# Optimization experiments

Measured on AMD Instinct MI355X. Metric: run time of the kernel, lower is better.

Reference implementation:

```python
import jax, jax.numpy as jnp
import numpy as np

PROTO_DIM = 512
PROTO_NUM = 4096
BSZ = 256
SUBTEXT_NUM = 64
TEMP = 0.9


def setup_inputs() -> dict:
    key = jax.random.key(0)
    k1, k2, k3 = jax.random.split(key, 3)
    subtexts = jax.random.normal(k1, (BSZ, SUBTEXT_NUM, PROTO_DIM), dtype=jnp.float32)
    prototype = jax.random.normal(k2, (PROTO_NUM, PROTO_DIM), dtype=jnp.float32)
    uniform = jax.random.uniform(k3, (BSZ * SUBTEXT_NUM, PROTO_NUM), dtype=jnp.float32)
    return {"subtexts": subtexts, "prototype": prototype, "uniform": uniform}


def reference(subtexts, prototype, uniform):
    # flatten: [N, D] with N = bsz * subtext_num
    flatten = subtexts.reshape(-1, PROTO_DIM)
    # dist: [N, proto_num] = flatten @ prototype.T
    dist = jnp.einsum("nd,pd->np", flatten, prototype)
    # Gumbel noise g = -log(-log(u)), matching torch F.gumbel_softmax sampling
    tiny = jnp.float32(1e-10)
    gumbel = -jnp.log(-jnp.log(uniform + tiny) + tiny)
    # noisy logits -> softmax over codebook dim (tau = curr_temp)
    soft_one_hot = jax.nn.softmax((dist + gumbel) / jnp.float32(TEMP), axis=1)
    # output: [N, D] soft codebook lookup
    output = jnp.einsum("np,pd->nd", soft_one_hot, prototype)
    proto_idx = jnp.argmax(soft_one_hot, axis=1)
    proto_loss = jnp.mean(jnp.abs(output - flatten))
    return (output, proto_loss, proto_idx)
```

## Files before the change

kernel.cpp:

```cpp
#include <hip/hip_runtime.h>
#include <math.h>

#define NROWS 16384
#define DIM   512
#define NPROTO 4096
#define TINV (1.0f / 0.9f)
#define LOSS_OFF ((size_t)NROWS * DIM)
#define IDX_OFF  ((size_t)NROWS * DIM + 1)

typedef __attribute__((ext_vector_type(8))) short short8;
typedef __attribute__((ext_vector_type(4))) float f32x4;

__global__ void zero_loss_kernel(float* out) { out[LOSS_OFF] = 0.0f; }

static __device__ __forceinline__ unsigned short f2bf(float x) {
    unsigned u = __float_as_uint(x);
    u = (u + 0x7fffu + ((u >> 16) & 1u)) >> 16;
    return (unsigned short)u;
}
static __device__ __forceinline__ float bf2f(unsigned short b) {
    return __uint_as_float(((unsigned)b) << 16);
}
static __device__ __forceinline__ void gl_lds16(const void* g, void* l) {
    __builtin_amdgcn_global_load_lds((const __attribute__((address_space(1))) unsigned int*)g,
                                     (__attribute__((address_space(3))) unsigned int*)l, 16, 0, 0);
}

__global__ __launch_bounds__(256)
void split_bf16_kernel(const float* __restrict__ src, unsigned short* __restrict__ dhi,
                       unsigned short* __restrict__ dmid, int nrows)
{
    __shared__ __align__(16) unsigned short shi[64][520];
    __shared__ __align__(16) unsigned short smid[64][520];
    const int tid = threadIdx.x;
    const int r0 = blockIdx.x * 64;
#pragma unroll
    for (int q = 0; q < 32; ++q) {
        int idx = q * 256 + tid;
        int row = idx >> 7;
        int k4 = (idx & 127) << 2;
        float4 v = *(const float4*)&src[(size_t)(r0 + row) * DIM + k4];
        unsigned short h0 = f2bf(v.x), h1 = f2bf(v.y), h2 = f2bf(v.z), h3 = f2bf(v.w);
        shi[row][k4] = h0; shi[row][k4 + 1] = h1; shi[row][k4 + 2] = h2; shi[row][k4 + 3] = h3;
        smid[row][k4]     = f2bf(v.x - bf2f(h0));
        smid[row][k4 + 1] = f2bf(v.y - bf2f(h1));
        smid[row][k4 + 2] = f2bf(v.z - bf2f(h2));
        smid[row][k4 + 3] = f2bf(v.w - bf2f(h3));
    }
    __syncthreads();
    const int row = tid & 63;
#pragma unroll
    for (int i = 0; i < 16; ++i) {
        int c = i * 4 + (tid >> 6);
        size_t o = (size_t)c * nrows + r0 + row;
        ((ulonglong2*)dhi)[o]  = *(const ulonglong2*)&shi[row][c * 8];
        ((ulonglong2*)dmid)[o] = *(const ulonglong2*)&smid[row][c * 8];
    }
}

#define BM 32
#define BN 256
#define NCHUNK (NPROTO / BN)
#define NT 16
#define CAP 80
#define PRUNE_AT 56
#define THRH 12.0f

__global__ __launch_bounds__(256, 2)
void attr_proto_mfma(const float* __restrict__ A, const float* __restrict__ Pr,
                     const float* __restrict__ U, float* __restrict__ out,
                     const unsigned short* __restrict__ wsAhi, const unsigned short* __restrict__ wsAmid,
                     const unsigned short* __restrict__ wsPhi, const unsigned short* __restrict__ wsPmid)
{
    __shared__ __align__(16) unsigned short sA[2][4][BM][8];
    __shared__ __align__(16) unsigned short sP[2][4][BN][8];
    __shared__ float hZ[BM][CAP];
    __shared__ unsigned short hI[BM][CAP];
    __shared__ int cnt[BM];
    __shared__ float mRun[BM], lRun[BM];
    __shared__ float wMax[4][BM], wSum[4][BM];
    __shared__ float epZ[8][BM];
    __shared__ int epI[8][BM];
    __shared__ int pruneFlag;

    const int tid = threadIdx.x;
    const int w = tid >> 6;
    const int lane = tid & 63;
    const int l4 = lane & 15;
    const int lh = lane >> 4;
    const int row0 = blockIdx.x * BM;

    for (int r = tid; r < BM; r += 256) { cnt[r] = 0; mRun[r] = -1e30f; lRun[r] = 0.f; }
    if (tid == 0) pruneFlag = 0;

    const unsigned short* gp[9];
    int str9[9];
    int fx9[9];
    unsigned short* ld9[9];
#pragma unroll
    for (int si = 0; si < 9; ++si) {
        int s = w * 9 + si;
        if (s < 4) {
            int sp = s >> 1, gpair = s & 1;
            int g = gpair * 2 + (lane >> 5);
            gp[si]  = (sp ? wsAmid : wsAhi) + ((size_t)g * NROWS + row0 + (lane & 31)) * 8;
            str9[si] = 4 * NROWS * 8;
            fx9[si]  = -16 * 4 * NROWS * 8;
            ld9[si] = &sA[sp][gpair * 2][0][0] + (size_t)lane * 8;
        } else {
            int p = s - 4;
            int sp = p >> 4, rem = p & 15, g = rem >> 2, q = rem & 3;
            gp[si]  = (sp ? wsPmid : wsPhi) + ((size_t)g * NPROTO + q * 64 + lane) * 8;
            str9[si] = 4 * NPROTO * 8;
            fx9[si]  = -16 * 4 * NPROTO * 8 + BN * 8;
            ld9[si] = &sP[sp][g][q * 64][0] + (size_t)lane * 8;
        }
    }
#define DO_STAGE() { _Pragma("unroll") for (int si = 0; si < 9; ++si) { gl_lds16(gp[si], ld9[si]); gp[si] += str9[si]; } }

    DO_STAGE();
    __syncthreads();

    for (int ch = 0; ch < NCHUNK; ++ch) {
        const int pbase = ch * BN;
        f32x4 acc[2][4];
#pragma unroll
        for (int mf = 0; mf < 2; ++mf)
#pragma unroll
            for (int nf = 0; nf < 4; ++nf) { acc[mf][nf][0]=0.f; acc[mf][nf][1]=0.f; acc[mf][nf][2]=0.f; acc[mf][nf][3]=0.f; }

#pragma unroll 2
        for (int t = 0; t < NT; ++t) {
            if (t > 0) {
                __syncthreads();
                DO_STAGE();
                __syncthreads();
            }
            short8 a[2][2], b[4][2];
#pragma unroll
            for (int mf = 0; mf < 2; ++mf) {
                a[mf][0] = *(const short8*)&sA[0][lh][mf * 16 + l4][0];
                a[mf][1] = *(const short8*)&sA[1][lh][mf * 16 + l4][0];
            }
#pragma unroll
            for (int nf = 0; nf < 4; ++nf) {
                b[nf][0] = *(const short8*)&sP[0][lh][w * 64 + nf * 16 + l4][0];
                b[nf][1] = *(const short8*)&sP[1][lh][w * 64 + nf * 16 + l4][0];
            }
#pragma unroll
            for (int mf = 0; mf < 2; ++mf)
#pragma unroll
                for (int nf = 0; nf < 4; ++nf) {
                    acc[mf][nf] = __builtin_amdgcn_mfma_f32_16x16x32_bf16(a[mf][0], b[nf][0], acc[mf][nf], 0, 0, 0);
                    acc[mf][nf] = __builtin_amdgcn_mfma_f32_16x16x32_bf16(a[mf][0], b[nf][1], acc[mf][nf], 0, 0, 0);
                    acc[mf][nf] = __builtin_amdgcn_mfma_f32_16x16x32_bf16(a[mf][1], b[nf][0], acc[mf][nf], 0, 0, 0);
                }
        }
        __syncthreads();
        if (ch + 1 < NCHUNK) {
#pragma unroll
            for (int si = 0; si < 9; ++si) gp[si] += fx9[si];
            DO_STAGE();
        }

#pragma unroll
        for (int mf = 0; mf < 2; ++mf) {
            float uu[16];
            const int rb = row0 + mf * 16 + lh * 4;
#pragma unroll
            for (int nf = 0; nf < 4; ++nf)
#pragma unroll
                for (int r = 0; r < 4; ++r)
                    uu[nf * 4 + r] = U[(size_t)(rb + r) * NPROTO + pbase + w * 64 + nf * 16 + l4];
#pragma unroll
            for (int nf = 0; nf < 4; ++nf)
#pragma unroll
                for (int r = 0; r < 4; ++r) {
                    float g = -__logf(-__logf(uu[nf * 4 + r] + 1e-10f) + 1e-10f);
                    acc[mf][nf][r] = (acc[mf][nf][r] + g) * TINV;
                }
        }
#pragma unroll
        for (int mf = 0; mf < 2; ++mf) {
            f32x4 rm;
#pragma unroll
            for (int r = 0; r < 4; ++r)
                rm[r] = fmaxf(fmaxf(acc[mf][0][r], acc[mf][1][r]), fmaxf(acc[mf][2][r], acc[mf][3][r]));
#pragma unroll
            for (int off = 1; off < 16; off <<= 1)
#pragma unroll
                for (int r = 0; r < 4; ++r) rm[r] = fmaxf(rm[r], __shfl_xor(rm[r], off));
            if (l4 == 0)
#pragma unroll
                for (int r = 0; r < 4; ++r) wMax[w][mf * 16 + lh * 4 + r] = rm[r];
        }
        __syncthreads();
#pragma unroll
        for (int mf = 0; mf < 2; ++mf) {
#pragma unroll
            for (int r = 0; r < 4; ++r) {
                const int rl = mf * 16 + lh * 4 + r;
                float gm = fmaxf(fmaxf(wMax[0][rl], wMax[1][rl]), fmaxf(wMax[2][rl], wMax[3][rl]));
                float mn = fmaxf(mRun[rl], gm);
                float s = 0.f;
#pragma unroll
                for (int nf = 0; nf < 4; ++nf) s += __expf(acc[mf][nf][r] - mn);
#pragma unroll
                for (int off = 1; off < 16; off <<= 1) s += __shfl_xor(s, off);
                if (l4 == 0) wSum[w][rl] = s;
                float thrv = mn - THRH;
#pragma unroll
                for (int nf = 0; nf < 4; ++nf) {
                    float z = acc[mf][nf][r];
                    if (z > thrv) {
                        int pos = atomicAdd(&cnt[rl], 1);
                        if (pos < CAP) { hZ[rl][pos] = z; hI[rl][pos] = (unsigned short)(pbase + w * 64 + nf * 16 + l4); }
                    }
                }
            }
        }
        __syncthreads();
        if (tid < BM) {
            float gm = fmaxf(fmaxf(wMax[0][tid], wMax[1][tid]), fmaxf(wMax[2][tid], wMax[3][tid]));
            float mn = fmaxf(mRun[tid], gm);
            float S = wSum[0][tid] + wSum[1][tid] + wSum[2][tid] + wSum[3][tid];
            lRun[tid] = lRun[tid] * __expf(mRun[tid] - mn) + S;
            mRun[tid] = mn;
            if (cnt[tid] > PRUNE_AT) atomicOr(&pruneFlag, 1);
        }
        __syncthreads();
        if (pruneFlag) {
            for (int r = 0; r < BM; ++r) {
                int c0 = min(cnt[r], CAP);
                if (c0 > PRUNE_AT) {
                    float thr2 = mRun[r] - THRH;
                    float ez = 0.f; int ei = 0; bool keep = false;
                    if (tid < c0) { ez = hZ[r][tid]; ei = hI[r][tid]; keep = ez > thr2; }
                    __syncthreads();
                    if (tid == 0) cnt[r] = 0;
                    __syncthreads();
                    if (keep) { int pos = atomicAdd(&cnt[r], 1); hZ[r][pos] = ez; hI[r][pos] = (unsigned short)ei; }
                    __syncthreads();
                }
            }
            if (tid == 0) pruneFlag = 0;
        }
        __syncthreads();
    }

    __syncthreads();
    const int rq = tid & 31;
    const int qq = tid >> 5;
    {
        const int c = min(cnt[rq], CAP);
        float qm = -1e30f;
        for (int e = qq; e < c; e += 8) qm = fmaxf(qm, hZ[rq][e]);
        epZ[qq][rq] = qm;
    }
    __syncthreads();
    {
        const int c = min(cnt[rq], CAP);
        float bzr = epZ[0][rq];
#pragma unroll
        for (int q = 1; q < 8; ++q) bzr = fmaxf(bzr, epZ[q][rq]);
        const float win = bzr - 3.0f;
        float bestz = -1e30f; int bestp = 1 << 30;
        const float* ap = &A[(size_t)(row0 + rq) * DIM];
        for (int e = qq; e < c; e += 8) {
            if (hZ[rq][e] > win) {
                const int p = hI[rq][e];
                const float* pp = &Pr[(size_t)p * DIM];
                float d = 0.f;
                for (int k = 0; k < DIM; k += 4) {
                    float4 av = *(const float4*)&ap[k];
                    float4 pv = *(const float4*)&pp[k];
                    d = fmaf(av.x, pv.x, d);
                    d = fmaf(av.y, pv.y, d);
                    d = fmaf(av.z, pv.z, d);
                    d = fmaf(av.w, pv.w, d);
                }
                float u = U[(size_t)(row0 + rq) * NPROTO + p];
                float g = -logf(-logf(u + 1e-10f) + 1e-10f);
                float zz = (d + g) * (1.0f / 0.9f);
                if (zz > bestz || (zz == bestz && p < bestp)) { bestz = zz; bestp = p; }
            }
        }
        __syncthreads();
        epZ[qq][rq] = bestz;
        epI[qq][rq] = bestp;
    }
    __syncthreads();
    if (tid < BM) {
        float bz2 = epZ[0][tid]; int bp2 = epI[0][tid];
#pragma unroll
        for (int q = 1; q < 8; ++q) {
            float z = epZ[q][tid]; int p = epI[q][tid];
            if (z > bz2 || (z == bz2 && p < bp2)) { bz2 = z; bp2 = p; }
        }
        out[IDX_OFF + row0 + tid] = (float)bp2;
    }

    float lossAcc = 0.f;
    for (int r = w; r < BM; r += 4) {
        const int grow = row0 + r;
        const int c = min(cnt[r], CAP);
        const float mm = mRun[r];
        const float li = 1.0f / lRun[r];
        float o[8];
#pragma unroll
        for (int q = 0; q < 8; ++q) o[q] = 0.f;
        for (int e = 0; e < c; ++e) {
            float wgt = __expf(hZ[r][e] - mm) * li;
            const float* pp = &Pr[(size_t)hI[r][e] * DIM + lane * 8];
            float4 p0 = *(const float4*)pp;
            float4 p1 = *(const float4*)(pp + 4);
            o[0] += wgt * p0.x; o[1] += wgt * p0.y; o[2] += wgt * p0.z; o[3] += wgt * p0.w;
            o[4] += wgt * p1.x; o[5] += wgt * p1.y; o[6] += wgt * p1.z; o[7] += wgt * p1.w;
        }
        const float* fr = &A[(size_t)grow * DIM + lane * 8];
        float4 f0 = *(const float4*)fr; float4 f1 = *(const float4*)(fr + 4);
        *(float4*)&out[(size_t)grow * DIM + lane * 8]     = make_float4(o[0], o[1], o[2], o[3]);
        *(float4*)&out[(size_t)grow * DIM + lane * 8 + 4] = make_float4(o[4], o[5], o[6], o[7]);
        lossAcc += fabsf(o[0] - f0.x) + fabsf(o[1] - f0.y) + fabsf(o[2] - f0.z) + fabsf(o[3] - f0.w)
                 + fabsf(o[4] - f1.x) + fabsf(o[5] - f1.y) + fabsf(o[6] - f1.z) + fabsf(o[7] - f1.w);
    }
#pragma unroll
    for (int off = 1; off < 64; off <<= 1) lossAcc += __shfl_xor(lossAcc, off);
    if (lane == 0) atomicAdd(&out[LOSS_OFF], lossAcc * (1.0f / ((float)NROWS * (float)DIM)));
}

#define FCAP 192
#define FTHR 20.0f

__global__ __launch_bounds__(256, 1)
void attr_proto_fused_valu(const float* __restrict__ A, const float* __restrict__ Pr,
                           const float* __restrict__ U, float* __restrict__ out)
{
    __shared__ __align__(16) float As[64][64 + 4];
    __shared__ __align__(16) float Bs[128][64 + 4];
    __shared__ float hZ[64][FCAP];
    __shared__ unsigned short hI[64][FCAP];
    __shared__ int cnt[64];
    __shared__ float mArr[64];
    __shared__ float lArr[64];
    __shared__ int pruneFlag;

    const int tid = threadIdx.x;
    const int tx = tid & 31;
    const int ty = tid >> 5;
    const int row0 = blockIdx.x * 64;

    for (int r = tid; r < 64; r += 256) cnt[r] = 0;
    if (tid == 0) pruneFlag = 0;

    float m[8], l[8], bz[8];
    int bi[8];
#pragma unroll
    for (int i = 0; i < 8; ++i) { m[i] = -INFINITY; l[i] = 0.0f; bz[i] = -INFINITY; bi[i] = 0; }
    __syncthreads();

    for (int ch = 0; ch < 32; ++ch) {
        const int pbase = ch * 128;
        float acc[8][4];
#pragma unroll
        for (int i = 0; i < 8; ++i)
#pragma unroll
            for (int j = 0; j < 4; ++j) acc[i][j] = 0.0f;

        for (int kk = 0; kk < DIM; kk += 64) {
#pragma unroll
            for (int q = 0; q < 4; ++q) {
                int lin = tid + q * 256;
                int lr = lin >> 4; int kq = (lin & 15) << 2;
                *(float4*)&As[lr][kq] = *(const float4*)&A[(size_t)(row0 + lr) * DIM + kk + kq];
            }
#pragma unroll
            for (int q = 0; q < 8; ++q) {
                int lin = tid + q * 256;
                int pr = lin >> 4; int kq = (lin & 15) << 2;
                *(float4*)&Bs[pr][kq] = *(const float4*)&Pr[(size_t)(pbase + pr) * DIM + kk + kq];
            }
            __syncthreads();
#pragma unroll 4
            for (int k4 = 0; k4 < 64; k4 += 4) {
                float4 av[8], bv[4];
#pragma unroll
                for (int i = 0; i < 8; ++i) av[i] = *(const float4*)&As[ty * 8 + i][k4];
#pragma unroll
                for (int j = 0; j < 4; ++j) bv[j] = *(const float4*)&Bs[tx + 32 * j][k4];
#pragma unroll
                for (int i = 0; i < 8; ++i)
#pragma unroll
                    for (int j = 0; j < 4; ++j) {
                        acc[i][j] += av[i].x * bv[j].x; acc[i][j] += av[i].y * bv[j].y;
                        acc[i][j] += av[i].z * bv[j].z; acc[i][j] += av[i].w * bv[j].w;
                    }
            }
            __syncthreads();
        }
#pragma unroll
        for (int i = 0; i < 8; ++i) {
            const int ri = ty * 8 + i;
            const size_t urow = (size_t)(row0 + ri) * NPROTO + pbase;
            float z[4]; float lmax = -INFINITY;
#pragma unroll
            for (int j = 0; j < 4; ++j) {
                float u = U[urow + tx + 32 * j];
                float g = -logf(-logf(u + 1e-10f) + 1e-10f);
                z[j] = (acc[i][j] + g) * TINV;
                lmax = fmaxf(lmax, z[j]);
            }
#pragma unroll
            for (int off = 16; off; off >>= 1) lmax = fmaxf(lmax, __shfl_xor(lmax, off, 32));
            const float mn = fmaxf(m[i], lmax);
            float s = 0.0f;
#pragma unroll
            for (int j = 0; j < 4; ++j) s += expf(z[j] - mn);
#pragma unroll
            for (int off = 16; off; off >>= 1) s += __shfl_xor(s, off, 32);
            l[i] = l[i] * expf(m[i] - mn) + s;
            m[i] = mn;
#pragma unroll
            for (int j = 0; j < 4; ++j) {
                const int p = pbase + tx + 32 * j;
                if (z[j] > bz[i]) { bz[i] = z[j]; bi[i] = p; }
                if (z[j] > mn - FTHR) {
                    int pos = atomicAdd(&cnt[ri], 1);
                    if (pos < FCAP) { hZ[ri][pos] = z[j]; hI[ri][pos] = (unsigned short)p; }
                }
            }
            if (tx == 0) {
                mArr[ri] = mn;
                if (cnt[ri] > 64) atomicOr(&pruneFlag, 1);
            }
        }
        __syncthreads();
        if (pruneFlag) {
            for (int r = 0; r < 64; ++r) {
                const int c0 = min(cnt[r], FCAP);
                if (c0 > 64) {
                    const float thr = mArr[r] - FTHR;
                    float ez = 0.0f; int ei = 0; bool keep = false;
                    if (tid < c0) { ez = hZ[r][tid]; ei = hI[r][tid]; keep = (ez > thr); }
                    __syncthreads();
                    if (tid == 0) cnt[r] = 0;
                    __syncthreads();
                    if (keep) { int pos = atomicAdd(&cnt[r], 1); hZ[r][pos] = ez; hI[r][pos] = (unsigned short)ei; }
                    __syncthreads();
                }
            }
            if (tid == 0) pruneFlag = 0;
            __syncthreads();
        }
    }
#pragma unroll
    for (int i = 0; i < 8; ++i) {
        const int ri = ty * 8 + i;
        float vz = bz[i]; int vi = bi[i];
#pragma unroll
        for (int off = 16; off; off >>= 1) {
            float oz = __shfl_xor(vz, off, 32); int oi = __shfl_xor(vi, off, 32);
            if (oz > vz || (oz == vz && oi < vi)) { vz = oz; vi = oi; }
        }
        if (tx == 0) { lArr[ri] = l[i]; out[IDX_OFF + row0 + ri] = (float)vi; }
    }
    __syncthreads();

    const int wv = tid >> 6;
    const int lane = tid & 63;
    float lossAcc = 0.0f;
    for (int r = wv; r < 64; r += 4) {
        const int grow = row0 + r;
        const int c = min(cnt[r], FCAP);
        const float mm = mArr[r];
        const float li = 1.0f / lArr[r];
        float o[8];
#pragma unroll
        for (int q = 0; q < 8; ++q) o[q] = 0.0f;
        for (int e = 0; e < c; ++e) {
            const float wg = expf(hZ[r][e] - mm) * li;
            const float* pp = &Pr[(size_t)hI[r][e] * DIM + lane * 8];
            float4 p0 = *(const float4*)pp; float4 p1 = *(const float4*)(pp + 4);
            o[0] += wg * p0.x; o[1] += wg * p0.y; o[2] += wg * p0.z; o[3] += wg * p0.w;
            o[4] += wg * p1.x; o[5] += wg * p1.y; o[6] += wg * p1.z; o[7] += wg * p1.w;
        }
        const float* fr = &A[(size_t)grow * DIM + lane * 8];
        float4 f0 = *(const float4*)fr; float4 f1 = *(const float4*)(fr + 4);
        *(float4*)&out[(size_t)grow * DIM + lane * 8]     = make_float4(o[0], o[1], o[2], o[3]);
        *(float4*)&out[(size_t)grow * DIM + lane * 8 + 4] = make_float4(o[4], o[5], o[6], o[7]);
        lossAcc += fabsf(o[0]-f0.x) + fabsf(o[1]-f0.y) + fabsf(o[2]-f0.z) + fabsf(o[3]-f0.w)
                 + fabsf(o[4]-f1.x) + fabsf(o[5]-f1.y) + fabsf(o[6]-f1.z) + fabsf(o[7]-f1.w);
    }
#pragma unroll
    for (int off = 32; off; off >>= 1) lossAcc += __shfl_xor(lossAcc, off, 64);
    if (lane == 0) atomicAdd(&out[LOSS_OFF], lossAcc * (1.0f / ((float)NROWS * (float)DIM)));
}

extern "C" void kernel_launch(void* const* d_in, const int* in_sizes, int n_in,
                              void* d_out, int out_size, void* d_ws, size_t ws_size,
                              hipStream_t stream)
{
    const float* A  = (const float*)d_in[0];
    const float* Pr = (const float*)d_in[1];
    const float* U  = (const float*)d_in[2];
    float* out = (float*)d_out;

    const size_t NA = (size_t)NROWS * DIM;
    const size_t NP = (size_t)NPROTO * DIM;
    const size_t need = (2 * NA + 2 * NP) * sizeof(unsigned short);

    if (ws_size >= need) {
        unsigned short* wsAhi  = (unsigned short*)d_ws;
        unsigned short* wsAmid = wsAhi + NA;
        unsigned short* wsPhi  = wsAmid + NA;
        unsigned short* wsPmid = wsPhi + NP;
        split_bf16_kernel<<<NROWS / 64, 256, 0, stream>>>(A, wsAhi, wsAmid, NROWS);
        split_bf16_kernel<<<NPROTO / 64, 256, 0, stream>>>(Pr, wsPhi, wsPmid, NPROTO);
        zero_loss_kernel<<<1, 1, 0, stream>>>(out);
        attr_proto_mfma<<<NROWS / BM, 256, 0, stream>>>(A, Pr, U, out, wsAhi, wsAmid, wsPhi, wsPmid);
    } else {
        zero_loss_kernel<<<1, 1, 0, stream>>>(out);
        attr_proto_fused_valu<<<NROWS / 64, 256, 0, stream>>>(A, Pr, U, out);
    }
}
```

Measured before the change: 478.0 us.

## Switch distance GEMM to two-limb int8 MFMA with double-buffered LDS staging

Replaces the bf16 hi/mid split with per-row scaled two-limb int8 quantization, so the main GEMM runs on i8 MFMA with K=64 per instruction and half the staged bytes. LDS staging is double-buffered so each global->LDS load overlaps compute and needs one barrier per step instead of two. The candidate list moves to global memory with a larger cap and an online max only, and the softmax sum and argmax are rebuilt in the epilogue from that list. The quantized dist is less precise than the split-bf16 result, which is partly offset by the existing fp32 recheck for argmax. The larger workspace list adds global traffic.

```diff
diff --git a/kernel.cpp b/kernel.cpp
--- a/kernel.cpp
+++ b/kernel.cpp
@@ -7,81 +7,82 @@
 #define TINV (1.0f / 0.9f)
 #define LOSS_OFF ((size_t)NROWS * DIM)
 #define IDX_OFF  ((size_t)NROWS * DIM + 1)
-
-typedef __attribute__((ext_vector_type(8))) short short8;
+#define LCAP 128
+#define LTHR 10.0f
+
+typedef __attribute__((ext_vector_type(4))) int i32x4;
 typedef __attribute__((ext_vector_type(4))) float f32x4;
 
 __global__ void zero_loss_kernel(float* out) { out[LOSS_OFF] = 0.0f; }
 
-static __device__ __forceinline__ unsigned short f2bf(float x) {
-    unsigned u = __float_as_uint(x);
-    u = (u + 0x7fffu + ((u >> 16) & 1u)) >> 16;
-    return (unsigned short)u;
-}
-static __device__ __forceinline__ float bf2f(unsigned short b) {
-    return __uint_as_float(((unsigned)b) << 16);
-}
 static __device__ __forceinline__ void gl_lds16(const void* g, void* l) {
     __builtin_amdgcn_global_load_lds((const __attribute__((address_space(1))) unsigned int*)g,
                                      (__attribute__((address_space(3))) unsigned int*)l, 16, 0, 0);
 }
 
 __global__ __launch_bounds__(256)
-void split_bf16_kernel(const float* __restrict__ src, unsigned short* __restrict__ dhi,
-                       unsigned short* __restrict__ dmid, int nrows)
+void split_i8_kernel(const float* __restrict__ src, char* __restrict__ d1, char* __restrict__ d0,
+                     float* __restrict__ dScale, int nrows)
 {
-    __shared__ __align__(16) unsigned short shi[64][520];
-    __shared__ __align__(16) unsigned short smid[64][520];
+    __shared__ __align__(16) char s1[32][512];
+    __shared__ __align__(16) char s0[32][512];
     const int tid = threadIdx.x;
-    const int r0 = blockIdx.x * 64;
-#pragma unroll
-    for (int q = 0; q < 32; ++q) {
-        int idx = q * 256 + tid;
-        int row = idx >> 7;
-        int k4 = (idx & 127) << 2;
-        float4 v = *(const float4*)&src[(size_t)(r0 + row) * DIM + k4];
-        unsigned short h0 = f2bf(v.x), h1 = f2bf(v.y), h2 = f2bf(v.z), h3 = f2bf(v.w);
-        shi[row][k4] = h0; shi[row][k4 + 1] = h1; shi[row][k4 + 2] = h2; shi[row][k4 + 3] = h3;
-        smid[row][k4]     = f2bf(v.x - bf2f(h0));
-        smid[row][k4 + 1] = f2bf(v.y - bf2f(h1));
-        smid[row][k4 + 2] = f2bf(v.z - bf2f(h2));
-        smid[row][k4 + 3] = f2bf(v.w - bf2f(h3));
+    const int row = tid >> 3;
+    const int sub = tid & 7;
+    const int r0 = blockIdx.x * 32;
+    const float* rp = &src[(size_t)(r0 + row) * DIM + sub * 64];
+    float v[64];
+    float mx = 1e-20f;
+#pragma unroll
+    for (int i = 0; i < 16; ++i) {
+        float4 f = *(const float4*)&rp[i * 4];
+        v[i*4+0] = f.x; v[i*4+1] = f.y; v[i*4+2] = f.z; v[i*4+3] = f.w;
+        mx = fmaxf(mx, fmaxf(fmaxf(fabsf(f.x), fabsf(f.y)), fmaxf(fabsf(f.z), fabsf(f.w))));
+    }
+#pragma unroll
+    for (int off = 1; off < 8; off <<= 1) mx = fmaxf(mx, __shfl_xor(mx, off));
+    const float s   = mx * (1.0f / 16256.0f);
+    const float inv = 16256.0f / mx;
+    if (sub == 0) dScale[r0 + row] = s;
+#pragma unroll
+    for (int i = 0; i < 64; ++i) {
+        float q  = v[i] * inv;
+        float a1 = rintf(q * (1.0f / 128.0f));
+        float a0 = rintf(q - 128.0f * a1);
+        s1[row][sub * 64 + i] = (char)(int)a1;
+        s0[row][sub * 64 + i] = (char)(int)a0;
     }
     __syncthreads();
-    const int row = tid & 63;
-#pragma unroll
-    for (int i = 0; i < 16; ++i) {
-        int c = i * 4 + (tid >> 6);
-        size_t o = (size_t)c * nrows + r0 + row;
-        ((ulonglong2*)dhi)[o]  = *(const ulonglong2*)&shi[row][c * 8];
-        ((ulonglong2*)dmid)[o] = *(const ulonglong2*)&smid[row][c * 8];
+#pragma unroll
+    for (int i = 0; i < 4; ++i) {
+        int idx = i * 256 + tid;
+        int g = idx >> 5;
+        int rr = idx & 31;
+        size_t o = ((size_t)g * nrows + r0 + rr) * 16;
+        *(ulonglong2*)&d1[o] = *(const ulonglong2*)&s1[rr][g * 16];
+        *(ulonglong2*)&d0[o] = *(const ulonglong2*)&s0[rr][g * 16];
     }
 }
 
 #define BM 32
 #define BN 256
 #define NCHUNK (NPROTO / BN)
-#define NT 16
-#define CAP 80
-#define PRUNE_AT 56
-#define THRH 12.0f
+#define NT 8
 
 __global__ __launch_bounds__(256, 2)
-void attr_proto_mfma(const float* __restrict__ A, const float* __restrict__ Pr,
-                     const float* __restrict__ U, float* __restrict__ out,
-                     const unsigned short* __restrict__ wsAhi, const unsigned short* __restrict__ wsAmid,
-                     const unsigned short* __restrict__ wsPhi, const unsigned short* __restrict__ wsPmid)
+void attr_proto_i8(const float* __restrict__ A, const float* __restrict__ Pr,
+                   const float* __restrict__ U, float* __restrict__ out,
+                   uint2* __restrict__ gList,
+                   const char* __restrict__ wsA1, const char* __restrict__ wsA0,
+                   const char* __restrict__ wsP1, const char* __restrict__ wsP0,
+                   const float* __restrict__ wsSA, const float* __restrict__ wsSP)
 {
-    __shared__ __align__(16) unsigned short sA[2][4][BM][8];
-    __shared__ __align__(16) unsigned short sP[2][4][BN][8];
-    __shared__ float hZ[BM][CAP];
-    __shared__ unsigned short hI[BM][CAP];
+    __shared__ __align__(16) char sA[2][2][4][BM][16];
+    __shared__ __align__(16) char sP[2][2][4][BN][16];
+    __shared__ float wMax[4][BM];
+    __shared__ float mRun[BM];
+    __shared__ float smSA[BM];
     __shared__ int cnt[BM];
-    __shared__ float mRun[BM], lRun[BM];
-    __shared__ float wMax[4][BM], wSum[4][BM];
-    __shared__ float epZ[8][BM];
-    __shared__ int epI[8][BM];
-    __shared__ int pruneFlag;
 
     const int tid = threadIdx.x;
     const int w = tid >> 6;
@@ -90,94 +91,100 @@
     const int lh = lane >> 4;
     const int row0 = blockIdx.x * BM;
 
-    for (int r = tid; r < BM; r += 256) { cnt[r] = 0; mRun[r] = -1e30f; lRun[r] = 0.f; }
-    if (tid == 0) pruneFlag = 0;
-
-    const unsigned short* gp[9];
-    int str9[9];
-    int fx9[9];
-    unsigned short* ld9[9];
+    if (tid < BM) { mRun[tid] = -1e30f; cnt[tid] = 0; smSA[tid] = wsSA[row0 + tid]; }
+
+    const char* gp[9];
+    int str9[9], fx9[9], bstr9[9];
+    char* ld9[9];
 #pragma unroll
     for (int si = 0; si < 9; ++si) {
         int s = w * 9 + si;
         if (s < 4) {
-            int sp = s >> 1, gpair = s & 1;
+            int limb = s >> 1, gpair = s & 1;
             int g = gpair * 2 + (lane >> 5);
-            gp[si]  = (sp ? wsAmid : wsAhi) + ((size_t)g * NROWS + row0 + (lane & 31)) * 8;
-            str9[si] = 4 * NROWS * 8;
-            fx9[si]  = -16 * 4 * NROWS * 8;
-            ld9[si] = &sA[sp][gpair * 2][0][0] + (size_t)lane * 8;
+            gp[si]  = (limb ? wsA0 : wsA1) + ((size_t)g * NROWS + row0 + (lane & 31)) * 16;
+            str9[si] = 4 * NROWS * 16;
+            fx9[si]  = -NT * 4 * NROWS * 16;
+            ld9[si]  = &sA[0][limb][gpair * 2][0][0] + (size_t)lane * 16;
+            bstr9[si] = 2 * 4 * BM * 16;
         } else {
             int p = s - 4;
-            int sp = p >> 4, rem = p & 15, g = rem >> 2, q = rem & 3;
-            gp[si]  = (sp ? wsPmid : wsPhi) + ((size_t)g * NPROTO + q * 64 + lane) * 8;
-            str9[si] = 4 * NPROTO * 8;
-            fx9[si]  = -16 * 4 * NPROTO * 8 + BN * 8;
-            ld9[si] = &sP[sp][g][q * 64][0] + (size_t)lane * 8;
-        }
-    }
-#define DO_STAGE() { _Pragma("unroll") for (int si = 0; si < 9; ++si) { gl_lds16(gp[si], ld9[si]); gp[si] += str9[si]; } }
-
-    DO_STAGE();
+            int limb = p >> 4, rem = p & 15, g = rem >> 2, q = rem & 3;
+            gp[si]  = (limb ? wsP0 : wsP1) + ((size_t)g * NPROTO + q * 64 + lane) * 16;
+            str9[si] = 4 * NPROTO * 16;
+            fx9[si]  = -NT * 4 * NPROTO * 16 + BN * 16;
+            ld9[si]  = &sP[0][limb][g][q * 64][0] + (size_t)lane * 16;
+            bstr9[si] = 2 * 4 * BN * 16;
+        }
+    }
+#define DO_STAGE(b) { _Pragma("unroll") for (int si = 0; si < 9; ++si) { \
+        gl_lds16(gp[si], ld9[si] + ((b) ? bstr9[si] : 0)); gp[si] += str9[si]; } }
+#define DO_FIXUP() { _Pragma("unroll") for (int si = 0; si < 9; ++si) gp[si] += fx9[si]; }
+
+    i32x4 c11[2][4], c10[2][4], c01[2][4];
+    auto COMPUTE = [&](int cur) {
+        i32x4 a1[2], a0[2], b1[4], b0[4];
+#pragma unroll
+        for (int mf = 0; mf < 2; ++mf) {
+            a1[mf] = *(const i32x4*)&sA[cur][0][lh][mf * 16 + l4][0];
+            a0[mf] = *(const i32x4*)&sA[cur][1][lh][mf * 16 + l4][0];
+        }
+#pragma unroll
+        for (int nf = 0; nf < 4; ++nf) {
+            b1[nf] = *(const i32x4*)&sP[cur][0][lh][w * 64 + nf * 16 + l4][0];
+            b0[nf] = *(const i32x4*)&sP[cur][1][lh][w * 64 + nf * 16 + l4][0];
+        }
+#pragma unroll
+        for (int mf = 0; mf < 2; ++mf)
+#pragma unroll
+            for (int nf = 0; nf < 4; ++nf) {
+                c11[mf][nf] = __builtin_amdgcn_mfma_i32_16x16x64_i8(a1[mf], b1[nf], c11[mf][nf], 0, 0, 0);
+                c10[mf][nf] = __builtin_amdgcn_mfma_i32_16x16x64_i8(a1[mf], b0[nf], c10[mf][nf], 0, 0, 0);
+                c01[mf][nf] = __builtin_amdgcn_mfma_i32_16x16x64_i8(a0[mf], b1[nf], c01[mf][nf], 0, 0, 0);
+            }
+    };
+
+    DO_STAGE(0);
     __syncthreads();
 
     for (int ch = 0; ch < NCHUNK; ++ch) {
         const int pbase = ch * BN;
-        f32x4 acc[2][4];
+        float spv[4];
+#pragma unroll
+        for (int nf = 0; nf < 4; ++nf) spv[nf] = wsSP[pbase + w * 64 + nf * 16 + l4];
 #pragma unroll
         for (int mf = 0; mf < 2; ++mf)
 #pragma unroll
-            for (int nf = 0; nf < 4; ++nf) { acc[mf][nf][0]=0.f; acc[mf][nf][1]=0.f; acc[mf][nf][2]=0.f; acc[mf][nf][3]=0.f; }
+            for (int nf = 0; nf < 4; ++nf) {
+                c11[mf][nf] = i32x4{0,0,0,0}; c10[mf][nf] = i32x4{0,0,0,0}; c01[mf][nf] = i32x4{0,0,0,0};
+            }
 
 #pragma unroll 2
         for (int t = 0; t < NT; ++t) {
-            if (t > 0) {
-                __syncthreads();
-                DO_STAGE();
-                __syncthreads();
-            }
-            short8 a[2][2], b[4][2];
-#pragma unroll
-            for (int mf = 0; mf < 2; ++mf) {
-                a[mf][0] = *(const short8*)&sA[0][lh][mf * 16 + l4][0];
-                a[mf][1] = *(const short8*)&sA[1][lh][mf * 16 + l4][0];
-            }
-#pragma unroll
-            for (int nf = 0; nf < 4; ++nf) {
-                b[nf][0] = *(const short8*)&sP[0][lh][w * 64 + nf * 16 + l4][0];
-                b[nf][1] = *(const short8*)&sP[1][lh][w * 64 + nf * 16 + l4][0];
-            }
-#pragma unroll
-            for (int mf = 0; mf < 2; ++mf)
-#pragma unroll
-                for (int nf = 0; nf < 4; ++nf) {
-                    acc[mf][nf] = __builtin_amdgcn_mfma_f32_16x16x32_bf16(a[mf][0], b[nf][0], acc[mf][nf], 0, 0, 0);
-                    acc[mf][nf] = __builtin_amdgcn_mfma_f32_16x16x32_bf16(a[mf][0], b[nf][1], acc[mf][nf], 0, 0, 0);
-                    acc[mf][nf] = __builtin_amdgcn_mfma_f32_16x16x32_bf16(a[mf][1], b[nf][0], acc[mf][nf], 0, 0, 0);
-                }
-        }
-        __syncthreads();
-        if (ch + 1 < NCHUNK) {
-#pragma unroll
-            for (int si = 0; si < 9; ++si) gp[si] += fx9[si];
-            DO_STAGE();
-        }
-
+            const int cur = t & 1;
+            if (t < NT - 1) {
+                DO_STAGE(cur ^ 1);
+            } else if (ch + 1 < NCHUNK) {
+                DO_FIXUP(); DO_STAGE(cur ^ 1);
+            }
+            COMPUTE(cur);
+            __syncthreads();
+        }
+
+        f32x4 zf[2][4];
 #pragma unroll
         for (int mf = 0; mf < 2; ++mf) {
-            float uu[16];
             const int rb = row0 + mf * 16 + lh * 4;
 #pragma unroll
             for (int nf = 0; nf < 4; ++nf)
 #pragma unroll
-                for (int r = 0; r < 4; ++r)
-                    uu[nf * 4 + r] = U[(size_t)(rb + r) * NPROTO + pbase + w * 64 + nf * 16 + l4];
-#pragma unroll
-            for (int nf = 0; nf < 4; ++nf)
-#pragma unroll
                 for (int r = 0; r < 4; ++r) {
-                    float g = -__logf(-__logf(uu[nf * 4 + r] + 1e-10f) + 1e-10f);
-                    acc[mf][nf][r] = (acc[mf][nf][r] + g) * TINV;
+                    float dist = smSA[mf * 16 + lh * 4 + r] * spv[nf] *
+                                 (16384.0f * (float)c11[mf][nf][r] +
+                                  128.0f * ((float)c10[mf][nf][r] + (float)c01[mf][nf][r]));
+                    float u = U[(size_t)(rb + r) * NPROTO + pbase + w * 64 + nf * 16 + l4];
+                    float g = -__logf(-__logf(u + 1e-10f) + 1e-10f);
+                    zf[mf][nf][r] = (dist + g) * TINV;
                 }
         }
 #pragma unroll
@@ -185,90 +192,75 @@
             f32x4 rm;
 #pragma unroll
             for (int r = 0; r < 4; ++r)
-                rm[r] = fmaxf(fmaxf(acc[mf][0][r], acc[mf][1][r]), fmaxf(acc[mf][2][r], acc[mf][3][r]));
+                rm[r] = fmaxf(fmaxf(zf[mf][0][r], zf[mf][1][r]), fmaxf(zf[mf][2][r], zf[mf][3][r]));
 #pragma unroll
             for (int off = 1; off < 16; off <<= 1)
 #pragma unroll
                 for (int r = 0; r < 4; ++r) rm[r] = fmaxf(rm[r], __shfl_xor(rm[r], off));
-            if (l4 == 0)
-#pragma unroll
-                for (int r = 0; r < 4; ++r) wMax[w][mf * 16 + lh * 4 + r] = rm[r];
-        }
-        __syncthreads();
-#pragma unroll
-        for (int mf = 0; mf < 2; ++mf) {
 #pragma unroll
             for (int r = 0; r < 4; ++r) {
                 const int rl = mf * 16 + lh * 4 + r;
-                float gm = fmaxf(fmaxf(wMax[0][rl], wMax[1][rl]), fmaxf(wMax[2][rl], wMax[3][rl]));
-                float mn = fmaxf(mRun[rl], gm);
-                float s = 0.f;
-#pragma unroll
-                for (int nf = 0; nf < 4; ++nf) s += __expf(acc[mf][nf][r] - mn);
-#pragma unroll
-                for (int off = 1; off < 16; off <<= 1) s += __shfl_xor(s, off);
-                if (l4 == 0) wSum[w][rl] = s;
-                float thrv = mn - THRH;
+                float thrv = fmaxf(mRun[rl], rm[r]) - LTHR;
 #pragma unroll
                 for (int nf = 0; nf < 4; ++nf) {
-                    float z = acc[mf][nf][r];
+                    float z = zf[mf][nf][r];
                     if (z > thrv) {
                         int pos = atomicAdd(&cnt[rl], 1);
-                        if (pos < CAP) { hZ[rl][pos] = z; hI[rl][pos] = (unsigned short)(pbase + w * 64 + nf * 16 + l4); }
+                        if (pos < LCAP) {
+                            uint2 en; en.x = __float_as_uint(z); en.y = (unsigned)(pbase + w * 64 + nf * 16 + l4);
+                            gList[(size_t)(row0 + rl) * LCAP + pos] = en;
+                        }
                     }
                 }
             }
+            if (l4 == 0)
+#pragma unroll
+                for (int r = 0; r < 4; ++r) wMax[w][mf * 16 + lh * 4 + r] = rm[r];
         }
         __syncthreads();
         if (tid < BM) {
             float gm = fmaxf(fmaxf(wMax[0][tid], wMax[1][tid]), fmaxf(wMax[2][tid], wMax[3][tid]));
-            float mn = fmaxf(mRun[tid], gm);
-            float S = wSum[0][tid] + wSum[1][tid] + wSum[2][tid] + wSum[3][tid];
-            lRun[tid] = lRun[tid] * __expf(mRun[tid] - mn) + S;
-            mRun[tid] = mn;
-            if (cnt[tid] > PRUNE_AT) atomicOr(&pruneFlag, 1);
+            mRun[tid] = fmaxf(mRun[tid], gm);
         }
         __syncthreads();
-        if (pruneFlag) {
-            for (int r = 0; r < BM; ++r) {
-                int c0 = min(cnt[r], CAP);
-                if (c0 > PRUNE_AT) {
-                    float thr2 = mRun[r] - THRH;
-                    float ez = 0.f; int ei = 0; bool keep = false;
-                    if (tid < c0) { ez = hZ[r][tid]; ei = hI[r][tid]; keep = ez > thr2; }
-                    __syncthreads();
-                    if (tid == 0) cnt[r] = 0;
-                    __syncthreads();
-                    if (keep) { int pos = atomicAdd(&cnt[r], 1); hZ[r][pos] = ez; hI[r][pos] = (unsigned short)ei; }
-                    __syncthreads();
-                }
-            }
-            if (tid == 0) pruneFlag = 0;
-        }
-        __syncthreads();
-    }
+    }
+#undef DO_STAGE
+#undef DO_FIXUP
 
     __syncthreads();
-    const int rq = tid & 31;
-    const int qq = tid >> 5;
-    {
-        const int c = min(cnt[rq], CAP);
-        float qm = -1e30f;
-        for (int e = qq; e < c; e += 8) qm = fmaxf(qm, hZ[rq][e]);
-        epZ[qq][rq] = qm;
-    }
-    __syncthreads();
-    {
-        const int c = min(cnt[rq], CAP);
-        float bzr = epZ[0][rq];
-#pragma unroll
-        for (int q = 1; q < 8; ++q) bzr = fmaxf(bzr, epZ[q][rq]);
-        const float win = bzr - 3.0f;
+    float lossTot = 0.f;
+    for (int r = w; r < BM; r += 4) {
+        const int row = row0 + r;
+        const int c = min(cnt[r], LCAP);
+        const uint2* lst = &gList[(size_t)row * LCAP];
+
+        float M = -1e30f;
+        for (int e = lane; e < c; e += 64) M = fmaxf(M, __uint_as_float(lst[e].x));
+#pragma unroll
+        for (int off = 1; off < 64; off <<= 1) M = fmaxf(M, __shfl_xor(M, off));
+        const float cutoff = M - LTHR;
+
+        float L = 0.f, bz = -1e30f; int bi = 1 << 30;
+        for (int e = lane; e < c; e += 64) {
+            float z = __uint_as_float(lst[e].x); int p = (int)lst[e].y;
+            if (z > cutoff) {
+                L += __expf(z - M);
+                if (z > bz || (z == bz && p < bi)) { bz = z; bi = p; }
+            }
+        }
+#pragma unroll
+        for (int off = 1; off < 64; off <<= 1) {
+            L += __shfl_xor(L, off);
+            float oz = __shfl_xor(bz, off); int oi = __shfl_xor(bi, off);
+            if (oz > bz || (oz == bz && oi < bi)) { bz = oz; bi = oi; }
+        }
+
         float bestz = -1e30f; int bestp = 1 << 30;
-        const float* ap = &A[(size_t)(row0 + rq) * DIM];
-        for (int e = qq; e < c; e += 8) {
-            if (hZ[rq][e] > win) {
-                const int p = hI[rq][e];
+        const float* ap = &A[(size_t)row * DIM];
+        for (int e = lane; e < c; e += 64) {
+            float z = __uint_as_float(lst[e].x);
+            if (z > bz - 3.0f) {
+                int p = (int)lst[e].y;
                 const float* pp = &Pr[(size_t)p * DIM];
                 float d = 0.f;
                 for (int k = 0; k < DIM; k += 4) {
@@ -279,54 +271,45 @@
                     d = fmaf(av.z, pv.z, d);
                     d = fmaf(av.w, pv.w, d);
                 }
-                float u = U[(size_t)(row0 + rq) * NPROTO + p];
+                float u = U[(size_t)row * NPROTO + p];
                 float g = -logf(-logf(u + 1e-10f) + 1e-10f);
                 float zz = (d + g) * (1.0f / 0.9f);
                 if (zz > bestz || (zz == bestz && p < bestp)) { bestz = zz; bestp = p; }
             }
         }
-        __syncthreads();
-        epZ[qq][rq] = bestz;
-        epI[qq][rq] = bestp;
-    }
-    __syncthreads();
-    if (tid < BM) {
-        float bz2 = epZ[0][tid]; int bp2 = epI[0][tid];
-#pragma unroll
-        for (int q = 1; q < 8; ++q) {
-            float z = epZ[q][tid]; int p = epI[q][tid];
-            if (z > bz2 || (z == bz2 && p < bp2)) { bz2 = z; bp2 = p; }
-        }
-        out[IDX_OFF + row0 + tid] = (float)bp2;
-    }
-
-    float lossAcc = 0.f;
-    for (int r = w; r < BM; r += 4) {
-        const int grow = row0 + r;
-        const int c = min(cnt[r], CAP);
-        const float mm = mRun[r];
-        const float li = 1.0f / lRun[r];
+#pragma unroll
+        for (int off = 1; off < 64; off <<= 1) {
+            float oz = __shfl_xor(bestz, off); int oi = __shfl_xor(bestp, off);
+            if (oz > bestz || (oz == bestz && oi < bestp)) { bestz = oz; bestp = oi; }
+        }
+        if (lane == 0) out[IDX_OFF + row] = (float)bestp;
+
         float o[8];
 #pragma unroll
         for (int q = 0; q < 8; ++q) o[q] = 0.f;
+        const float Li = 1.0f / L;
         for (int e = 0; e < c; ++e) {
-            float wgt = __expf(hZ[r][e] - mm) * li;
-            const float* pp = &Pr[(size_t)hI[r][e] * DIM + lane * 8];
-            float4 p0 = *(const float4*)pp;
-            float4 p1 = *(const float4*)(pp + 4);
-            o[0] += wgt * p0.x; o[1] += wgt * p0.y; o[2] += wgt * p0.z; o[3] += wgt * p0.w;
-            o[4] += wgt * p1.x; o[5] += wgt * p1.y; o[6] += wgt * p1.z; o[7] += wgt * p1.w;
-        }
-        const float* fr = &A[(size_t)grow * DIM + lane * 8];
+            uint2 en = lst[e];
+            float z = __uint_as_float(en.x);
+            if (z > cutoff) {
+                float wgt = __expf(z - M) * Li;
+                const float* pp = &Pr[(size_t)en.y * DIM + lane * 8];
+                float4 p0 = *(const float4*)pp;
+                float4 p1 = *(const float4*)(pp + 4);
+                o[0] += wgt * p0.x; o[1] += wgt * p0.y; o[2] += wgt * p0.z; o[3] += wgt * p0.w;
+                o[4] += wgt * p1.x; o[5] += wgt * p1.y; o[6] += wgt * p1.z; o[7] += wgt * p1.w;
+            }
+        }
+        const float* fr = &A[(size_t)row * DIM + lane * 8];
         float4 f0 = *(const float4*)fr; float4 f1 = *(const float4*)(fr + 4);
-        *(float4*)&out[(size_t)grow * DIM + lane * 8]     = make_float4(o[0], o[1], o[2], o[3]);
-        *(float4*)&out[(size_t)grow * DIM + lane * 8 + 4] = make_float4(o[4], o[5], o[6], o[7]);
-        lossAcc += fabsf(o[0] - f0.x) + fabsf(o[1] - f0.y) + fabsf(o[2] - f0.z) + fabsf(o[3] - f0.w)
-                 + fabsf(o[4] - f1.x) + fabsf(o[5] - f1.y) + fabsf(o[6] - f1.z) + fabsf(o[7] - f1.w);
-    }
-#pragma unroll
-    for (int off = 1; off < 64; off <<= 1) lossAcc += __shfl_xor(lossAcc, off);
-    if (lane == 0) atomicAdd(&out[LOSS_OFF], lossAcc * (1.0f / ((float)NROWS * (float)DIM)));
+        *(float4*)&out[(size_t)row * DIM + lane * 8]     = make_float4(o[0], o[1], o[2], o[3]);
+        *(float4*)&out[(size_t)row * DIM + lane * 8 + 4] = make_float4(o[4], o[5], o[6], o[7]);
+        lossTot += fabsf(o[0]-f0.x) + fabsf(o[1]-f0.y) + fabsf(o[2]-f0.z) + fabsf(o[3]-f0.w)
+                 + fabsf(o[4]-f1.x) + fabsf(o[5]-f1.y) + fabsf(o[6]-f1.z) + fabsf(o[7]-f1.w);
+    }
+#pragma unroll
+    for (int off = 1; off < 64; off <<= 1) lossTot += __shfl_xor(lossTot, off);
+    if (lane == 0) atomicAdd(&out[LOSS_OFF], lossTot * (1.0f / ((float)NROWS * (float)DIM)));
 }
 
 #define FCAP 192
@@ -505,21 +488,28 @@
     const float* U  = (const float*)d_in[2];
     float* out = (float*)d_out;
 
-    const size_t NA = (size_t)NROWS * DIM;
-    const size_t NP = (size_t)NPROTO * DIM;
-    const size_t need = (2 * NA + 2 * NP) * sizeof(unsigned short);
+    const size_t szA = (size_t)NROWS * DIM;
+    const size_t szP = (size_t)NPROTO * DIM;
+    const size_t scABytes = (size_t)NROWS * sizeof(float);
+    const size_t scPBytes = (size_t)NPROTO * sizeof(float);
+    const size_t listBytes = (size_t)NROWS * LCAP * sizeof(uint2);
+    const size_t need = 2 * szA + 2 * szP + scABytes + scPBytes + listBytes;
+
+    zero_loss_kernel<<<1, 1, 0, stream>>>(out);
 
     if (ws_size >= need) {
-        unsigned short* wsAhi  = (unsigned short*)d_ws;
-        unsigned short* wsAmid = wsAhi + NA;
-        unsigned short* wsPhi  = wsAmid + NA;
-        unsigned short* wsPmid = wsPhi + NP;
-        split_bf16_kernel<<<NROWS / 64, 256, 0, stream>>>(A, wsAhi, wsAmid, NROWS);
-        split_bf16_kernel<<<NPROTO / 64, 256, 0, stream>>>(Pr, wsPhi, wsPmid, NPROTO);
-        zero_loss_kernel<<<1, 1, 0, stream>>>(out);
-        attr_proto_mfma<<<NROWS / BM, 256, 0, stream>>>(A, Pr, U, out, wsAhi, wsAmid, wsPhi, wsPmid);
+        char*  wsA1 = (char*)d_ws;
+        char*  wsA0 = wsA1 + szA;
+        char*  wsP1 = wsA0 + szA;
+        char*  wsP0 = wsP1 + szP;
+        float* wsSA = (float*)(wsP0 + szP);
+        float* wsSP = wsSA + NROWS;
+        uint2* gList = (uint2*)((char*)(wsSP + NPROTO));
+        split_i8_kernel<<<NROWS / 32, 256, 0, stream>>>(A, wsA1, wsA0, wsSA, NROWS);
+        split_i8_kernel<<<NPROTO / 32, 256, 0, stream>>>(Pr, wsP1, wsP0, wsSP, NPROTO);
+        attr_proto_i8<<<NROWS / BM, 256, 0, stream>>>(A, Pr, U, out, gList,
+                                                      wsA1, wsA0, wsP1, wsP0, wsSA, wsSP);
     } else {
-        zero_loss_kernel<<<1, 1, 0, stream>>>(out);
         attr_proto_fused_valu<<<NROWS / 64, 256, 0, stream>>>(A, Pr, U, out);
     }
 }
```

Result: faster. 455.7 us (-4.7%).
